# Kernel optimization log

Hardware: AMD Instinct MI355X
Metric: run time of the kernel (lower is better)

## Reference

```python
import jax, jax.numpy as jnp
import numpy as np

NUM_HEADS = 12


def setup_inputs() -> dict:
    key = jax.random.key(0)
    ks = jax.random.split(key, 6)
    B, F, P, C = 2, 8, 196, 768
    N = 1 + F * P
    s = 0.02
    return {
        "x": jax.random.normal(ks[0], (B, N, C), jnp.float32),
        "Wqkv": jax.random.normal(ks[1], (C, 3 * C), jnp.float32) * s,
        "Wq": jax.random.normal(ks[2], (C, C), jnp.float32) * s,
        "Wkv": jax.random.normal(ks[3], (C, 2 * C), jnp.float32) * s,
        "Wproj": jax.random.normal(ks[4], (C, C), jnp.float32) * s,
        "bproj": jnp.zeros((C,), jnp.float32),
        "seq_len": 196,
        "num_frames": 8,
    }


def reference(x, Wqkv, Wq, Wkv, Wproj, bproj, seq_len, num_frames):
    B, N, C = x.shape
    H = NUM_HEADS
    d = C // H
    scale = d ** -0.5
    F, P = num_frames, seq_len
    S = F * P  # N == 1 + S

    qkv = x @ Wqkv                                # [B, N, 3C]
    q, k, v = jnp.split(qkv, 3, axis=-1)
    def to_heads(t):  # [B, N, C] -> [B*H, N, d]
        return t.reshape(B, N, H, d).transpose(0, 2, 1, 3).reshape(B * H, N, d)
    q, k, v = to_heads(q), to_heads(k), to_heads(v)

    # --- cls token attends over everything ---
    cls_q = q[:, :1] * scale                      # [BH, 1, d]
    cls_attn = jax.nn.softmax(jnp.einsum('bid,bjd->bij', cls_q, k), axis=-1)
    cls_out = jnp.einsum('bij,bjd->bid', cls_attn, v)  # [BH, 1, d]
    cls_out = cls_out.reshape(B, H, d).reshape(B, 1, C)

    # --- per-frame spatial softmax ---
    q_, k_, v_ = q[:, 1:], k[:, 1:], v[:, 1:]     # [BH, S, d]
    qk = jnp.einsum('bqd,bkd->bqk', q_, k_).reshape(B * H, S, F, P)
    sp_attn = jax.nn.softmax(scale * qk, axis=-1)  # softmax over patches within frame
    v_f = v_.reshape(B * H, F, P, d)
    xt = jnp.einsum('bqfn,bfnd->bqfd', sp_attn, v_f)  # [BH, S, F, d]

    x4 = xt.reshape(B, H, S, F, d).transpose(0, 2, 3, 1, 4).reshape(B, S, F, C)

    # --- diagonal extraction: query frame g == key frame f ---
    x5 = x4.reshape(B, F, P, F, C)
    xd = jnp.diagonal(x5, axis1=1, axis2=3)       # [B, P, C, F]
    xd = xd.transpose(0, 3, 1, 2).reshape(B, S, C)

    # --- temporal trajectory attention ---
    q2 = (xd @ Wq).reshape(B, S, H, d).transpose(0, 2, 1, 3) * scale  # [B,H,S,d]
    kv2 = x4 @ Wkv                                # [B, S, F, 2C]
    k2 = kv2[..., :C].reshape(B, S, F, H, d).transpose(0, 3, 1, 2, 4)  # [B,H,S,F,d]
    attn2 = jax.nn.softmax(jnp.einsum('bhsd,bhsfd->bhsf', q2, k2), axis=-1)
    # use_original_code=True: aggregate the trajectory tensor x4 itself
    xr = x4.reshape(B, S, F, H, d).transpose(0, 3, 1, 2, 4)            # [B,H,S,F,d]
    out = jnp.einsum('bhsf,bhsfd->bhsd', attn2, xr)
    out = out.transpose(0, 2, 1, 3).reshape(B, S, C)

    out = jnp.concatenate([cls_out, out], axis=1) @ Wproj + bproj      # [B, N, C]
    return out, attn2
```

## Files before the change

kernel.cpp:

```cpp
#include <hip/hip_runtime.h>

namespace {
constexpr int kB = 2;
constexpr int kH = 12;
constexpr int kD = 64;
constexpr int kC = 768;
constexpr int kF = 8;
constexpr int kP = 196;
constexpr int kS = kF * kP;
constexpr int kN = 1 + kS;
constexpr int k3C = 3 * kC;
constexpr float kScale = 0.125f;
constexpr int kBH = kB * kH;
constexpr int kPpad = 224;
constexpr int kLpad = 1600;
}

typedef __attribute__((ext_vector_type(8))) short bf16x8;
typedef __attribute__((ext_vector_type(4))) float f32x4;
typedef __attribute__((ext_vector_type(4))) unsigned int u32x4;

__device__ inline ushort f2bf(float x) {
  union { float f; unsigned u; } v{x};
  unsigned r = v.u + 0x7fff + ((v.u >> 16) & 1);
  return (ushort)(r >> 16);
}
__device__ inline float bf2f(ushort u) {
  union { unsigned u; float f; } v{(unsigned)u << 16};
  return v.f;
}

__device__ __forceinline__ void gload_lds16(const void* g, void* l) {
  __builtin_amdgcn_global_load_lds(
      (const __attribute__((address_space(1))) unsigned int*)g,
      (__attribute__((address_space(3))) unsigned int*)l, 16, 0, 0);
}

__device__ inline void storeC(float v, float* p) { *p = v; }
__device__ inline void storeC(float v, ushort* p) { *p = f2bf(v); }

template <typename OutT>
__global__ __launch_bounds__(256) void gemm_bf16(
    const ushort* __restrict__ A, const ushort* __restrict__ Bt,
    const float* __restrict__ bias, OutT* __restrict__ C,
    int M, int N, int K, int nbx) {
  const int nwg = gridDim.x;
  const int q = nwg >> 3, rr = nwg & 7;
  const int xcd = blockIdx.x & 7, loc = blockIdx.x >> 3;
  const int vid = ((xcd < rr) ? xcd * (q + 1) : rr * (q + 1) + (xcd - rr) * q) + loc;
  const int m0 = (vid / nbx) * 128, n0 = (vid % nbx) * 128;

  __shared__ __align__(16) ushort As[128 * 32];
  __shared__ __align__(16) ushort Bs[128 * 32];
  const int tid = threadIdx.x;
  const int r0 = tid >> 2, c0 = tid & 3;
  const int r1 = r0 + 64;
  const int sc0 = (c0 ^ ((r0 >> 1) & 3)) * 8;
  const int sc1 = (c0 ^ ((r1 >> 1) & 3)) * 8;
  const int ar0 = min(m0 + r0, M - 1), ar1 = min(m0 + r1, M - 1);
  const ushort* ga0 = A + (size_t)ar0 * K + sc0;
  const ushort* ga1 = A + (size_t)ar1 * K + sc1;
  const ushort* gb0 = Bt + (size_t)(n0 + r0) * K + sc0;
  const ushort* gb1 = Bt + (size_t)(n0 + r1) * K + sc1;
  const int w = tid >> 6;
  char* lA0 = (char*)As + w * 1024;
  char* lA1 = (char*)As + 4096 + w * 1024;
  char* lB0 = (char*)Bs + w * 1024;
  char* lB1 = (char*)Bs + 4096 + w * 1024;
  const int lane = tid & 63;
  const int lr = lane & 15, lg = lane >> 4;
  const int wr = w >> 1, wc = w & 1;
  f32x4 acc[4][4] = {};
  for (int kt = 0; kt < K; kt += 32) {
    gload_lds16(ga0 + kt, lA0);
    gload_lds16(ga1 + kt, lA1);
    gload_lds16(gb0 + kt, lB0);
    gload_lds16(gb1 + kt, lB1);
    __syncthreads();
    bf16x8 af[4], bfr[4];
#pragma unroll
    for (int m = 0; m < 4; ++m) {
      int row = wr * 64 + m * 16 + lr;
      int ch = lg ^ ((row >> 1) & 3);
      af[m] = *(const bf16x8*)(As + row * 32 + ch * 8);
    }
#pragma unroll
    for (int n = 0; n < 4; ++n) {
      int row = wc * 64 + n * 16 + lr;
      int ch = lg ^ ((row >> 1) & 3);
      bfr[n] = *(const bf16x8*)(Bs + row * 32 + ch * 8);
    }
#pragma unroll
    for (int m = 0; m < 4; ++m)
#pragma unroll
      for (int n = 0; n < 4; ++n)
        acc[m][n] =
            __builtin_amdgcn_mfma_f32_16x16x32_bf16(af[m], bfr[n], acc[m][n], 0, 0, 0);
    __syncthreads();
  }
#pragma unroll
  for (int m = 0; m < 4; ++m) {
#pragma unroll
    for (int r = 0; r < 4; ++r) {
      const int mg = m0 + wr * 64 + m * 16 + lg * 4 + r;
      if (mg < M) {
        OutT* crow = C + (size_t)mg * N + n0 + wc * 64 + lr;
#pragma unroll
        for (int n = 0; n < 4; ++n) {
          float v = acc[m][n][r];
          if (bias) v += bias[n0 + wc * 64 + n * 16 + lr];
          storeC(v, crow + n * 16);
        }
      }
    }
  }
}

__global__ void pack_x_k(const float* __restrict__ X, ushort* __restrict__ Xb,
                         int n4) {
  const int i = blockIdx.x * 256 + threadIdx.x;
  if (i >= n4) return;
  float4 v = ((const float4*)X)[i];
  ushort4 o = {f2bf(v.x), f2bf(v.y), f2bf(v.z), f2bf(v.w)};
  ((ushort4*)Xb)[i] = o;
}

__global__ __launch_bounds__(256) void pack_wt_k(const float* __restrict__ W,
                                                 ushort* __restrict__ Wt,
                                                 int ldw) {
  __shared__ float t[32][33];
  const int nb = blockIdx.x * 32;
  const int kb = blockIdx.y * 32;
  const int tx = threadIdx.x & 31, ty = threadIdx.x >> 5;
#pragma unroll
  for (int i = 0; i < 32; i += 8)
    t[ty + i][tx] = W[(size_t)(kb + ty + i) * ldw + nb + tx];
  __syncthreads();
#pragma unroll
  for (int i = 0; i < 32; i += 8)
    Wt[(size_t)(nb + ty + i) * 768 + kb + tx] = f2bf(t[tx][ty + i]);
}

__global__ void pack_qk_k(const float* __restrict__ qkv, ushort* __restrict__ Qb,
                          ushort* __restrict__ Kb) {
  const int idx = blockIdx.x * 256 + threadIdx.x;
  if (idx >= kBH * kS * kD) return;
  const int j = idx & 63;
  const int s = (idx >> 6) % kS;
  const int bh = idx / (kS * kD);
  const int b = bh / kH, h = bh % kH;
  const size_t src = (size_t)(b * kN + 1 + s) * k3C + h * kD + j;
  Qb[idx] = f2bf(qkv[src] * kScale);
  Kb[idx] = f2bf(qkv[src + kC]);
}

__global__ void pack_vt_k(const float* __restrict__ qkv, ushort* __restrict__ Vt) {
  const int idx = blockIdx.x * 256 + threadIdx.x;
  if (idx >= kBH * kF * kD * kPpad) return;
  const int n = idx % kPpad;
  const int j = (idx / kPpad) & 63;
  const int f = (idx / (kPpad * kD)) & 7;
  const int bh = idx / (kPpad * kD * kF);
  const int b = bh / kH, h = bh % kH;
  float v = 0.f;
  if (n < kP)
    v = qkv[(size_t)(b * kN + 1 + f * kP + n) * k3C + 2 * kC + h * kD + j];
  Vt[idx] = f2bf(v);
}

__global__ __launch_bounds__(256) void sp_attn_mfma(
    const ushort* __restrict__ Qb, const ushort* __restrict__ Kb,
    const ushort* __restrict__ Vt, ushort* __restrict__ x4b) {
  const int w = threadIdx.x >> 6;
  const int lane = threadIdx.x & 63;
  const int fbh = blockIdx.x;
  const int f = fbh / 24, bh = fbh % 24;
  const int tile = blockIdx.y * 4 + w;
  if (tile >= 49) return;
  const int q0 = tile * 32;
  const int lr = lane & 15;
  const int lg = lane >> 4;

  const ushort* qrow = Qb + ((size_t)bh * kS + q0 + lr) * kD + lg * 8;
  const bf16x8 a00 = *(const bf16x8*)qrow;
  const bf16x8 a01 = *(const bf16x8*)(qrow + 32);
  const bf16x8 a10 = *(const bf16x8*)(qrow + 16 * kD);
  const bf16x8 a11 = *(const bf16x8*)(qrow + 16 * kD + 32);

  f32x4 s0[13], s1[13];
  const ushort* kbase = Kb + ((size_t)bh * kS + f * kP + lr) * kD + lg * 8;
#pragma unroll
  for (int nt = 0; nt < 13; ++nt) {
    const ushort* kr = kbase + (size_t)nt * 16 * kD;
    bf16x8 b0 = *(const bf16x8*)kr;
    bf16x8 b1 = *(const bf16x8*)(kr + 32);
    f32x4 acc0 = {0.f, 0.f, 0.f, 0.f}, acc1 = {0.f, 0.f, 0.f, 0.f};
    acc0 = __builtin_amdgcn_mfma_f32_16x16x32_bf16(b0, a00, acc0, 0, 0, 0);
    acc0 = __builtin_amdgcn_mfma_f32_16x16x32_bf16(b1, a01, acc0, 0, 0, 0);
    acc1 = __builtin_amdgcn_mfma_f32_16x16x32_bf16(b0, a10, acc1, 0, 0, 0);
    acc1 = __builtin_amdgcn_mfma_f32_16x16x32_bf16(b1, a11, acc1, 0, 0, 0);
    s0[nt] = acc0;
    s1[nt] = acc1;
  }
  if (lg >= 1) {
#pragma unroll
    for (int r = 0; r < 4; ++r) { s0[12][r] = -1e30f; s1[12][r] = -1e30f; }
  }

  float m0 = -1e30f, m1 = -1e30f;
#pragma unroll
  for (int nt = 0; nt < 13; ++nt)
#pragma unroll
    for (int r = 0; r < 4; ++r) {
      m0 = fmaxf(m0, s0[nt][r]);
      m1 = fmaxf(m1, s1[nt][r]);
    }
  m0 = fmaxf(m0, __shfl_xor(m0, 16));
  m0 = fmaxf(m0, __shfl_xor(m0, 32));
  m1 = fmaxf(m1, __shfl_xor(m1, 16));
  m1 = fmaxf(m1, __shfl_xor(m1, 32));

  float sum0 = 0.f, sum1 = 0.f;
  u32x4 breg0[7], breg1[7];
#pragma unroll
  for (int blk = 0; blk < 7; ++blk) {
    unsigned pk0[2][2], pk1[2][2];
#pragma unroll
    for (int t = 0; t < 2; ++t) {
      const int nt = blk * 2 + t;
      if (nt < 13) {
        float e0 = __expf(s0[nt][0] - m0), e1 = __expf(s0[nt][1] - m0);
        float e2 = __expf(s0[nt][2] - m0), e3 = __expf(s0[nt][3] - m0);
        sum0 += (e0 + e1) + (e2 + e3);
        pk0[t][0] = ((unsigned)f2bf(e1) << 16) | f2bf(e0);
        pk0[t][1] = ((unsigned)f2bf(e3) << 16) | f2bf(e2);
        float g0 = __expf(s1[nt][0] - m1), g1 = __expf(s1[nt][1] - m1);
        float g2 = __expf(s1[nt][2] - m1), g3 = __expf(s1[nt][3] - m1);
        sum1 += (g0 + g1) + (g2 + g3);
        pk1[t][0] = ((unsigned)f2bf(g1) << 16) | f2bf(g0);
        pk1[t][1] = ((unsigned)f2bf(g3) << 16) | f2bf(g2);
      } else {
        pk0[t][0] = 0; pk0[t][1] = 0;
        pk1[t][0] = 0; pk1[t][1] = 0;
      }
    }
#pragma unroll
    for (int j2 = 0; j2 < 4; ++j2) {
      const int srcLane = ((lg & 1) * 2 + (j2 >> 1)) * 16 + lr;
      unsigned t0 = (unsigned)__shfl((int)pk0[0][j2 & 1], srcLane);
      unsigned t1 = (unsigned)__shfl((int)pk0[1][j2 & 1], srcLane);
      breg0[blk][j2] = (lg < 2) ? t0 : t1;
      unsigned u0 = (unsigned)__shfl((int)pk1[0][j2 & 1], srcLane);
      unsigned u1 = (unsigned)__shfl((int)pk1[1][j2 & 1], srcLane);
      breg1[blk][j2] = (lg < 2) ? u0 : u1;
    }
  }
  sum0 += __shfl_xor(sum0, 16);
  sum0 += __shfl_xor(sum0, 32);
  sum1 += __shfl_xor(sum1, 16);
  sum1 += __shfl_xor(sum1, 32);
  const float inv0 = 1.f / sum0, inv1 = 1.f / sum1;

  const ushort* vbase = Vt + ((size_t)(bh * kF + f) * kD + lr) * kPpad + lg * 8;
  f32x4 o0[4] = {}, o1[4] = {};
#pragma unroll
  for (int nt2 = 0; nt2 < 4; ++nt2) {
    const ushort* vb = vbase + (size_t)nt2 * 16 * kPpad;
#pragma unroll
    for (int blk = 0; blk < 7; ++blk) {
      bf16x8 av = *(const bf16x8*)(vb + blk * 32);
      bf16x8 pb0 = __builtin_bit_cast(bf16x8, breg0[blk]);
      bf16x8 pb1 = __builtin_bit_cast(bf16x8, breg1[blk]);
      o0[nt2] = __builtin_amdgcn_mfma_f32_16x16x32_bf16(av, pb0, o0[nt2], 0, 0, 0);
      o1[nt2] = __builtin_amdgcn_mfma_f32_16x16x32_bf16(av, pb1, o1[nt2], 0, 0, 0);
    }
  }

  const int b = bh / kH, h = bh % kH;
  const size_t base0 =
      ((size_t)(b * kS + q0 + lr) * kF + f) * kC + h * kD + lg * 4;
#pragma unroll
  for (int nt2 = 0; nt2 < 4; ++nt2) {
    ushort4 v0, v1;
    v0.x = f2bf(o0[nt2][0] * inv0);
    v0.y = f2bf(o0[nt2][1] * inv0);
    v0.z = f2bf(o0[nt2][2] * inv0);
    v0.w = f2bf(o0[nt2][3] * inv0);
    *(ushort4*)(x4b + base0 + nt2 * 16) = v0;
    v1.x = f2bf(o1[nt2][0] * inv1);
    v1.y = f2bf(o1[nt2][1] * inv1);
    v1.z = f2bf(o1[nt2][2] * inv1);
    v1.w = f2bf(o1[nt2][3] * inv1);
    *(ushort4*)(x4b + base0 + (size_t)16 * kF * kC + nt2 * 16) = v1;
  }
}

__global__ __launch_bounds__(256) void cls_logits_k(const float* __restrict__ qkv,
                                                    float* __restrict__ logits) {
  const int chunk = blockIdx.x, bh = blockIdx.y;
  const int b = bh / kH, h = bh % kH;
  const int g = threadIdx.x & 15, row = threadIdx.x >> 4;
  const size_t base = (size_t)b * kN * k3C;
  float4 q4 = *(const float4*)(qkv + base + h * kD + g * 4);
  q4.x *= kScale; q4.y *= kScale; q4.z *= kScale; q4.w *= kScale;
#pragma unroll
  for (int i = 0; i < 16; ++i) {
    const int n = chunk * 256 + i * 16 + row;
    if (n < kN) {
      const float4 kv =
          *(const float4*)(qkv + base + (size_t)n * k3C + kC + h * kD + g * 4);
      float p = q4.x * kv.x + q4.y * kv.y + q4.z * kv.z + q4.w * kv.w;
#pragma unroll
      for (int o = 8; o; o >>= 1) p += __shfl_xor(p, o, 16);
      if (g == 0) logits[bh * kLpad + n] = p;
    }
  }
}

__global__ __launch_bounds__(256) void cls_softmax_k(const float* __restrict__ logits,
                                                     float* __restrict__ pbuf) {
  __shared__ float red[8];
  const int bh = blockIdx.x, tid = threadIdx.x;
  float m = -1e30f;
  for (int n = tid; n < kN; n += 256) m = fmaxf(m, logits[bh * kLpad + n]);
#pragma unroll
  for (int o = 32; o; o >>= 1) m = fmaxf(m, __shfl_xor(m, o));
  if ((tid & 63) == 0) red[tid >> 6] = m;
  __syncthreads();
  m = fmaxf(fmaxf(red[0], red[1]), fmaxf(red[2], red[3]));
  float sum = 0.f;
  for (int n = tid; n < kN; n += 256) sum += __expf(logits[bh * kLpad + n] - m);
#pragma unroll
  for (int o = 32; o; o >>= 1) sum += __shfl_xor(sum, o);
  if ((tid & 63) == 0) red[4 + (tid >> 6)] = sum;
  __syncthreads();
  const float inv = 1.f / (red[4] + red[5] + red[6] + red[7]);
  for (int n = tid; n < kN; n += 256)
    pbuf[bh * kLpad + n] = __expf(logits[bh * kLpad + n] - m) * inv;
}

__global__ __launch_bounds__(256) void cls_pv_k(const float* __restrict__ qkv,
                                                const float* __restrict__ pbuf,
                                                float* __restrict__ partial) {
  __shared__ float pb[256];
  const int chunk = blockIdx.x, bh = blockIdx.y;
  const int b = bh / kH, h = bh % kH;
  const int j = threadIdx.x & 63, part = threadIdx.x >> 6;
  const size_t base = (size_t)b * kN * k3C + 2 * kC + h * kD + j;
  float acc = 0.f;
#pragma unroll 4
  for (int i = 0; i < 64; ++i) {
    const int n = chunk * 256 + i * 4 + part;
    if (n < kN) acc = fmaf(pbuf[bh * kLpad + n], qkv[base + (size_t)n * k3C], acc);
  }
  pb[threadIdx.x] = acc;
  __syncthreads();
  if (part == 0)
    partial[((size_t)bh * 7 + chunk) * kD + j] =
        pb[j] + pb[64 + j] + pb[128 + j] + pb[192 + j];
}

__global__ void cls_red_k(const float* __restrict__ partial,
                          ushort* __restrict__ xin_b) {
  const int bh = blockIdx.x, j = threadIdx.x;
  const int b = bh / kH, h = bh % kH;
  float s = 0.f;
#pragma unroll
  for (int c = 0; c < 7; ++c) s += partial[((size_t)bh * 7 + c) * kD + j];
  xin_b[(size_t)(b * kN) * kC + h * kD + j] = f2bf(s);
}

__global__ void xd_gather_k(const ushort* __restrict__ x4b,
                            ushort* __restrict__ xd_b) {
  const int idx = blockIdx.x * 256 + threadIdx.x;
  const int total = kB * kS * (kC / 8);
  if (idx >= total) return;
  const int row = idx / (kC / 8);
  const int cg = idx - row * (kC / 8);
  const int b = row / kS, s = row - b * kS;
  const int fq = s / kP;
  ((ulonglong2*)xd_b)[(size_t)row * (kC / 8) + cg] =
      ((const ulonglong2*)x4b)[((size_t)(b * kS + s) * kF + fq) * (kC / 8) + cg];
}

__global__ __launch_bounds__(256) void attn2_k(
    const ushort* __restrict__ q2b, const ushort* __restrict__ k2b,
    const ushort* __restrict__ x4b, ushort* __restrict__ xin_b,
    float* __restrict__ attn2out) {
  const int item = blockIdx.x * 4 + (threadIdx.x >> 6);
  const int lane = threadIdx.x & 63;
  const int s = item % kS;
  const int t = item / kS;
  const int h = t % kH, b = t / kH;
  const float qv = bf2f(q2b[(size_t)(b * kS + s) * kC + h * kD + lane]) * kScale;
  float l[kF];
#pragma unroll
  for (int f = 0; f < kF; ++f) {
    float p = qv * bf2f(k2b[((size_t)(b * kS + s) * kF + f) * kC + h * kD + lane]);
#pragma unroll
    for (int o = 32; o; o >>= 1) p += __shfl_xor(p, o);
    l[f] = p;
  }
  float m = l[0];
#pragma unroll
  for (int f = 1; f < kF; ++f) m = fmaxf(m, l[f]);
  float sum = 0.f;
#pragma unroll
  for (int f = 0; f < kF; ++f) {
    l[f] = __expf(l[f] - m);
    sum += l[f];
  }
  const float inv = 1.f / sum;
  float o = 0.f;
#pragma unroll
  for (int f = 0; f < kF; ++f)
    o = fmaf(l[f] * inv,
             bf2f(x4b[((size_t)(b * kS + s) * kF + f) * kC + h * kD + lane]), o);
  if (lane < kF)
    attn2out[((size_t)(b * kH + h) * kS + s) * kF + lane] = l[lane] * inv;
  xin_b[(size_t)(b * kN + 1 + s) * kC + h * kD + lane] = f2bf(o);
}

extern "C" void kernel_launch(void* const* d_in, const int* in_sizes, int n_in,
                              void* d_out, int out_size, void* d_ws,
                              size_t ws_size, hipStream_t stream) {
  const float* x = (const float*)d_in[0];
  const float* Wqkv = (const float*)d_in[1];
  const float* Wq = (const float*)d_in[2];
  const float* Wkv = (const float*)d_in[3];
  const float* Wproj = (const float*)d_in[4];
  const float* bproj = (const float*)d_in[5];

  char* p = (char*)d_ws;
  float* qkv = (float*)p;            p += (size_t)3138 * 2304 * 4;
  ushort* k2b = (ushort*)p;          p += (size_t)25088 * 768 * 2;
  ushort* q2b = (ushort*)p;          p += (size_t)3136 * 768 * 2;
  ushort* x4b = (ushort*)p;          p += (size_t)25088 * 768 * 2;
  ushort* xin_b = (ushort*)p;        p += (size_t)3138 * 768 * 2;
  ushort* xd_b = (ushort*)p;         p += (size_t)3136 * 768 * 2;
  ushort* xb = (ushort*)p;           p += (size_t)3138 * 768 * 2;
  ushort* Wqkv_t = (ushort*)p;       p += (size_t)2304 * 768 * 2;
  ushort* Wq_t = (ushort*)p;         p += (size_t)768 * 768 * 2;
  ushort* Wk_t = (ushort*)p;         p += (size_t)768 * 768 * 2;
  ushort* Wproj_t = (ushort*)p;      p += (size_t)768 * 768 * 2;
  ushort* Qb = (ushort*)p;           p += (size_t)kBH * kS * kD * 2;
  ushort* Kb = (ushort*)p;           p += ((size_t)kBH * kS + 16) * kD * 2;
  ushort* Vt = (ushort*)p;           p += (size_t)kBH * kF * kD * kPpad * 2;
  float* clsL = (float*)p;           p += (size_t)kBH * kLpad * 4;
  float* clsP = (float*)p;           p += (size_t)kBH * kLpad * 4;
  float* clsPart = (float*)p;

  float* out = (float*)d_out;
  float* attn2 = out + (size_t)kB * kN * kC;

  pack_x_k<<<(3138 * 768 / 4 + 255) / 256, 256, 0, stream>>>(x, xb, 3138 * 768 / 4);
  pack_wt_k<<<dim3(72, 24), 256, 0, stream>>>(Wqkv, Wqkv_t, 2304);
  pack_wt_k<<<dim3(24, 24), 256, 0, stream>>>(Wq, Wq_t, 768);
  pack_wt_k<<<dim3(24, 24), 256, 0, stream>>>(Wkv, Wk_t, 1536);
  pack_wt_k<<<dim3(24, 24), 256, 0, stream>>>(Wproj, Wproj_t, 768);
  gemm_bf16<float><<<18 * 25, 256, 0, stream>>>(xb, Wqkv_t, nullptr, qkv, 3138,
                                                2304, 768, 18);
  pack_qk_k<<<(kBH * kS * kD + 255) / 256, 256, 0, stream>>>(qkv, Qb, Kb);
  pack_vt_k<<<(kBH * kF * kD * kPpad + 255) / 256, 256, 0, stream>>>(qkv, Vt);
  cls_logits_k<<<dim3(7, 24), 256, 0, stream>>>(qkv, clsL);
  cls_softmax_k<<<24, 256, 0, stream>>>(clsL, clsP);
  cls_pv_k<<<dim3(7, 24), 256, 0, stream>>>(qkv, clsP, clsPart);
  cls_red_k<<<24, 64, 0, stream>>>(clsPart, xin_b);
  sp_attn_mfma<<<dim3(192, 13), 256, 0, stream>>>(Qb, Kb, Vt, x4b);
  xd_gather_k<<<(kB * kS * (kC / 8) + 255) / 256, 256, 0, stream>>>(x4b, xd_b);
  gemm_bf16<ushort><<<6 * 25, 256, 0, stream>>>(xd_b, Wq_t, nullptr, q2b, 3136,
                                                768, 768, 6);
  gemm_bf16<ushort><<<6 * 196, 256, 0, stream>>>(x4b, Wk_t, nullptr, k2b, 25088,
                                                 768, 768, 6);
  attn2_k<<<9408, 256, 0, stream>>>(q2b, k2b, x4b, xin_b, attn2);
  gemm_bf16<float><<<6 * 25, 256, 0, stream>>>(xin_b, Wproj_t, bproj, out, 3138,
                                               768, 768, 6);
}
```

Baseline: 281.6 us.

## Reassociate temporal attention logits via per-head q·Wk projection instead of K2 GEMM

The code no longer computes k2 = x4 @ Wk for all 25088 trajectory rows. It now projects each scaled query through the per-head slice of Wk, giving w2 of shape [B*S, H, C], and dots that with x4 inside a fused attention kernel. This removes the large 25088x768x768 GEMM and the k2 intermediate, and folds the scale into Wq during packing. In exchange it adds a per-head GEMM (3136x768 output per head with K=64), a large w2 buffer of about 58 MB written and then read back, and a fused kernel that stages x4 and w2 rows in LDS and does the logits with scalar FMAs.

```diff
diff --git a/kernel.cpp b/kernel.cpp
--- a/kernel.cpp
+++ b/kernel.cpp
@@ -14,6 +14,7 @@
 constexpr int kBH = kB * kH;
 constexpr int kPpad = 224;
 constexpr int kLpad = 1600;
+constexpr int kBS = kB * kS;
 }
 
 typedef __attribute__((ext_vector_type(8))) short bf16x8;
@@ -116,6 +117,80 @@
   }
 }
 
+__global__ __launch_bounds__(256) void w2_gemm(
+    const ushort* __restrict__ q2b, const ushort* __restrict__ Wkvb,
+    ushort* __restrict__ w2b) {
+  const int nwg = gridDim.x;
+  const int q = nwg >> 3, rr = nwg & 7;
+  const int xcd = blockIdx.x & 7, loc = blockIdx.x >> 3;
+  const int vid = ((xcd < rr) ? xcd * (q + 1) : rr * (q + 1) + (xcd - rr) * q) + loc;
+  const int h = vid / 150;
+  const int rem = vid - h * 150;
+  const int m0 = (rem / 6) * 128, n0 = (rem % 6) * 128;
+
+  __shared__ __align__(16) ushort As[128 * 32];
+  __shared__ __align__(16) ushort Bs[128 * 32];
+  const int tid = threadIdx.x;
+  const int r0 = tid >> 2, c0 = tid & 3;
+  const int r1 = r0 + 64;
+  const int sc0 = (c0 ^ ((r0 >> 1) & 3)) * 8;
+  const int sc1 = (c0 ^ ((r1 >> 1) & 3)) * 8;
+  const int ar0 = min(m0 + r0, kBS - 1), ar1 = min(m0 + r1, kBS - 1);
+  const ushort* ga0 = q2b + (size_t)ar0 * kC + h * 64 + sc0;
+  const ushort* ga1 = q2b + (size_t)ar1 * kC + h * 64 + sc1;
+  const ushort* gb0 = Wkvb + (size_t)(n0 + r0) * kC + h * 64 + sc0;
+  const ushort* gb1 = Wkvb + (size_t)(n0 + r1) * kC + h * 64 + sc1;
+  const int w = tid >> 6;
+  char* lA0 = (char*)As + w * 1024;
+  char* lA1 = (char*)As + 4096 + w * 1024;
+  char* lB0 = (char*)Bs + w * 1024;
+  char* lB1 = (char*)Bs + 4096 + w * 1024;
+  const int lane = tid & 63;
+  const int lr = lane & 15, lg = lane >> 4;
+  const int wr = w >> 1, wc = w & 1;
+  f32x4 acc[4][4] = {};
+#pragma unroll
+  for (int kt = 0; kt < 64; kt += 32) {
+    gload_lds16(ga0 + kt, lA0);
+    gload_lds16(ga1 + kt, lA1);
+    gload_lds16(gb0 + kt, lB0);
+    gload_lds16(gb1 + kt, lB1);
+    __syncthreads();
+    bf16x8 af[4], bfr[4];
+#pragma unroll
+    for (int m = 0; m < 4; ++m) {
+      int row = wr * 64 + m * 16 + lr;
+      int ch = lg ^ ((row >> 1) & 3);
+      af[m] = *(const bf16x8*)(As + row * 32 + ch * 8);
+    }
+#pragma unroll
+    for (int n = 0; n < 4; ++n) {
+      int row = wc * 64 + n * 16 + lr;
+      int ch = lg ^ ((row >> 1) & 3);
+      bfr[n] = *(const bf16x8*)(Bs + row * 32 + ch * 8);
+    }
+#pragma unroll
+    for (int m = 0; m < 4; ++m)
+#pragma unroll
+      for (int n = 0; n < 4; ++n)
+        acc[m][n] =
+            __builtin_amdgcn_mfma_f32_16x16x32_bf16(af[m], bfr[n], acc[m][n], 0, 0, 0);
+    __syncthreads();
+  }
+#pragma unroll
+  for (int m = 0; m < 4; ++m) {
+#pragma unroll
+    for (int r = 0; r < 4; ++r) {
+      const int mg = m0 + wr * 64 + m * 16 + lg * 4 + r;
+      if (mg < kBS) {
+        ushort* crow = w2b + (size_t)mg * (kH * kC) + h * kC + n0 + wc * 64 + lr;
+#pragma unroll
+        for (int n = 0; n < 4; ++n) crow[n * 16] = f2bf(acc[m][n][r]);
+      }
+    }
+  }
+}
+
 __global__ void pack_x_k(const float* __restrict__ X, ushort* __restrict__ Xb,
                          int n4) {
   const int i = blockIdx.x * 256 + threadIdx.x;
@@ -127,7 +202,7 @@
 
 __global__ __launch_bounds__(256) void pack_wt_k(const float* __restrict__ W,
                                                  ushort* __restrict__ Wt,
-                                                 int ldw) {
+                                                 int ldw, float scale) {
   __shared__ float t[32][33];
   const int nb = blockIdx.x * 32;
   const int kb = blockIdx.y * 32;
@@ -138,7 +213,17 @@
   __syncthreads();
 #pragma unroll
   for (int i = 0; i < 32; i += 8)
-    Wt[(size_t)(nb + ty + i) * 768 + kb + tx] = f2bf(t[tx][ty + i]);
+    Wt[(size_t)(nb + ty + i) * 768 + kb + tx] = f2bf(t[tx][ty + i] * scale);
+}
+
+__global__ void pack_wkv_k(const float* __restrict__ Wkv,
+                           ushort* __restrict__ Wkvb) {
+  const int i = blockIdx.x * 256 + threadIdx.x;
+  if (i >= 768 * 192) return;
+  const int c = i / 192, j4 = i - c * 192;
+  float4 v = *(const float4*)(Wkv + (size_t)c * 1536 + j4 * 4);
+  ushort4 o = {f2bf(v.x), f2bf(v.y), f2bf(v.z), f2bf(v.w)};
+  *(ushort4*)(Wkvb + (size_t)c * 768 + j4 * 4) = o;
 }
 
 __global__ void pack_qk_k(const float* __restrict__ qkv, ushort* __restrict__ Qb,
@@ -383,42 +468,70 @@
       ((const ulonglong2*)x4b)[((size_t)(b * kS + s) * kF + fq) * (kC / 8) + cg];
 }
 
-__global__ __launch_bounds__(256) void attn2_k(
-    const ushort* __restrict__ q2b, const ushort* __restrict__ k2b,
-    const ushort* __restrict__ x4b, ushort* __restrict__ xin_b,
-    float* __restrict__ attn2out) {
-  const int item = blockIdx.x * 4 + (threadIdx.x >> 6);
-  const int lane = threadIdx.x & 63;
-  const int s = item % kS;
-  const int t = item / kS;
-  const int h = t % kH, b = t / kH;
-  const float qv = bf2f(q2b[(size_t)(b * kS + s) * kC + h * kD + lane]) * kScale;
-  float l[kF];
-#pragma unroll
-  for (int f = 0; f < kF; ++f) {
-    float p = qv * bf2f(k2b[((size_t)(b * kS + s) * kF + f) * kC + h * kD + lane]);
-#pragma unroll
-    for (int o = 32; o; o >>= 1) p += __shfl_xor(p, o);
-    l[f] = p;
-  }
-  float m = l[0];
-#pragma unroll
-  for (int f = 1; f < kF; ++f) m = fmaxf(m, l[f]);
-  float sum = 0.f;
-#pragma unroll
-  for (int f = 0; f < kF; ++f) {
-    l[f] = __expf(l[f] - m);
-    sum += l[f];
-  }
-  const float inv = 1.f / sum;
-  float o = 0.f;
-#pragma unroll
-  for (int f = 0; f < kF; ++f)
-    o = fmaf(l[f] * inv,
-             bf2f(x4b[((size_t)(b * kS + s) * kF + f) * kC + h * kD + lane]), o);
-  if (lane < kF)
-    attn2out[((size_t)(b * kH + h) * kS + s) * kF + lane] = l[lane] * inv;
-  xin_b[(size_t)(b * kN + 1 + s) * kC + h * kD + lane] = f2bf(o);
+__global__ __launch_bounds__(256) void attn2_fused(
+    const ushort* __restrict__ x4b, const ushort* __restrict__ w2b,
+    ushort* __restrict__ xin_b, float* __restrict__ attn2out) {
+  __shared__ __align__(16) ushort x4s[kF * kC];
+  __shared__ __align__(16) ushort w2s[kH * kC];
+  const int bs = blockIdx.x;
+  const int b = bs / kS, s = bs - b * kS;
+  const int tid = threadIdx.x;
+  {
+    const ulonglong2* src = (const ulonglong2*)(x4b + (size_t)bs * kF * kC);
+    ulonglong2* dst = (ulonglong2*)x4s;
+    for (int i = tid; i < kF * kC / 8; i += 256) dst[i] = src[i];
+    const ulonglong2* srcw = (const ulonglong2*)(w2b + (size_t)bs * kH * kC);
+    ulonglong2* dstw = (ulonglong2*)w2s;
+    for (int i = tid; i < kH * kC / 8; i += 256) dstw[i] = srcw[i];
+  }
+  __syncthreads();
+  const int w = tid >> 6, lane = tid & 63;
+#pragma unroll
+  for (int hh = 0; hh < 3; ++hh) {
+    const int h = w * 3 + hh;
+    float part[kF] = {};
+#pragma unroll
+    for (int i = 0; i < 3; ++i) {
+      const int c = lane * 4 + i * 256;
+      ushort4 wv = *(const ushort4*)&w2s[h * kC + c];
+      const float w0 = bf2f(wv.x), w1 = bf2f(wv.y);
+      const float w2v = bf2f(wv.z), w3 = bf2f(wv.w);
+#pragma unroll
+      for (int f = 0; f < kF; ++f) {
+        ushort4 xv = *(const ushort4*)&x4s[f * kC + c];
+        part[f] += bf2f(xv.x) * w0 + bf2f(xv.y) * w1 + bf2f(xv.z) * w2v +
+                   bf2f(xv.w) * w3;
+      }
+    }
+    float l[kF];
+#pragma unroll
+    for (int f = 0; f < kF; ++f) {
+      float p = part[f];
+#pragma unroll
+      for (int o = 32; o; o >>= 1) p += __shfl_xor(p, o);
+      l[f] = p;
+    }
+    float m = l[0];
+#pragma unroll
+    for (int f = 1; f < kF; ++f) m = fmaxf(m, l[f]);
+    float sum = 0.f;
+#pragma unroll
+    for (int f = 0; f < kF; ++f) {
+      l[f] = __expf(l[f] - m);
+      sum += l[f];
+    }
+    const float inv = 1.f / sum;
+    float pv = 0.f;
+#pragma unroll
+    for (int f = 0; f < kF; ++f) pv = (lane == f) ? l[f] : pv;
+    if (lane < kF)
+      attn2out[((size_t)(b * kH + h) * kS + s) * kF + lane] = pv * inv;
+    float o = 0.f;
+#pragma unroll
+    for (int f = 0; f < kF; ++f)
+      o = fmaf(l[f] * inv, bf2f(x4s[f * kC + h * kD + lane]), o);
+    xin_b[(size_t)(b * kN + 1 + s) * kC + h * kD + lane] = f2bf(o);
+  }
 }
 
 extern "C" void kernel_launch(void* const* d_in, const int* in_sizes, int n_in,
@@ -433,15 +546,15 @@
 
   char* p = (char*)d_ws;
   float* qkv = (float*)p;            p += (size_t)3138 * 2304 * 4;
-  ushort* k2b = (ushort*)p;          p += (size_t)25088 * 768 * 2;
-  ushort* q2b = (ushort*)p;          p += (size_t)3136 * 768 * 2;
+  ushort* w2b = (ushort*)p;          p += (size_t)kBS * kH * kC * 2;
+  ushort* q2b = (ushort*)p;          p += (size_t)kBS * kC * 2;
   ushort* x4b = (ushort*)p;          p += (size_t)25088 * 768 * 2;
   ushort* xin_b = (ushort*)p;        p += (size_t)3138 * 768 * 2;
-  ushort* xd_b = (ushort*)p;         p += (size_t)3136 * 768 * 2;
+  ushort* xd_b = (ushort*)p;         p += (size_t)kBS * 768 * 2;
   ushort* xb = (ushort*)p;           p += (size_t)3138 * 768 * 2;
   ushort* Wqkv_t = (ushort*)p;       p += (size_t)2304 * 768 * 2;
   ushort* Wq_t = (ushort*)p;         p += (size_t)768 * 768 * 2;
-  ushort* Wk_t = (ushort*)p;         p += (size_t)768 * 768 * 2;
+  ushort* Wkvb = (ushort*)p;         p += (size_t)768 * 768 * 2;
   ushort* Wproj_t = (ushort*)p;      p += (size_t)768 * 768 * 2;
   ushort* Qb = (ushort*)p;           p += (size_t)kBH * kS * kD * 2;
   ushort* Kb = (ushort*)p;           p += ((size_t)kBH * kS + 16) * kD * 2;
@@ -454,10 +567,10 @@
   float* attn2 = out + (size_t)kB * kN * kC;
 
   pack_x_k<<<(3138 * 768 / 4 + 255) / 256, 256, 0, stream>>>(x, xb, 3138 * 768 / 4);
-  pack_wt_k<<<dim3(72, 24), 256, 0, stream>>>(Wqkv, Wqkv_t, 2304);
-  pack_wt_k<<<dim3(24, 24), 256, 0, stream>>>(Wq, Wq_t, 768);
-  pack_wt_k<<<dim3(24, 24), 256, 0, stream>>>(Wkv, Wk_t, 1536);
-  pack_wt_k<<<dim3(24, 24), 256, 0, stream>>>(Wproj, Wproj_t, 768);
+  pack_wt_k<<<dim3(72, 24), 256, 0, stream>>>(Wqkv, Wqkv_t, 2304, 1.f);
+  pack_wt_k<<<dim3(24, 24), 256, 0, stream>>>(Wq, Wq_t, 768, kScale);
+  pack_wkv_k<<<(768 * 192 + 255) / 256, 256, 0, stream>>>(Wkv, Wkvb);
+  pack_wt_k<<<dim3(24, 24), 256, 0, stream>>>(Wproj, Wproj_t, 768, 1.f);
   gemm_bf16<float><<<18 * 25, 256, 0, stream>>>(xb, Wqkv_t, nullptr, qkv, 3138,
                                                 2304, 768, 18);
   pack_qk_k<<<(kBH * kS * kD + 255) / 256, 256, 0, stream>>>(qkv, Qb, Kb);
@@ -468,11 +581,10 @@
   cls_red_k<<<24, 64, 0, stream>>>(clsPart, xin_b);
   sp_attn_mfma<<<dim3(192, 13), 256, 0, stream>>>(Qb, Kb, Vt, x4b);
   xd_gather_k<<<(kB * kS * (kC / 8) + 255) / 256, 256, 0, stream>>>(x4b, xd_b);
-  gemm_bf16<ushort><<<6 * 25, 256, 0, stream>>>(xd_b, Wq_t, nullptr, q2b, 3136,
+  gemm_bf16<ushort><<<6 * 25, 256, 0, stream>>>(xd_b, Wq_t, nullptr, q2b, kBS,
                                                 768, 768, 6);
-  gemm_bf16<ushort><<<6 * 196, 256, 0, stream>>>(x4b, Wk_t, nullptr, k2b, 25088,
-                                                 768, 768, 6);
-  attn2_k<<<9408, 256, 0, stream>>>(q2b, k2b, x4b, xin_b, attn2);
+  w2_gemm<<<1800, 256, 0, stream>>>(q2b, Wkvb, w2b);
+  attn2_fused<<<kBS, 256, 0, stream>>>(x4b, w2b, xin_b, attn2);
   gemm_bf16<float><<<6 * 25, 256, 0, stream>>>(xin_b, Wproj_t, bproj, out, 3138,
                                                768, 768, 6);
 }
```

New measurement: 266.7 us. -5.3%, faster.
